# Kernel optimization log

Hardware: AMD Instinct MI355X
Metric: run time of the kernel (lower is better)

## Reference

```python
import jax, jax.numpy as jnp
import numpy as np

T, B, F, H, P = 256, 512, 256, 512, 12  # seq len, batch, feature_dim, hidden_dim, p_interval


def setup_inputs() -> dict:
    key = jax.random.key(0)
    ks = jax.random.split(key, 9)
    s = 1.0 / np.sqrt(F + H)  # torch Linear default init scale
    def lin(k):
        kw, kb = jax.random.split(k)
        W = jax.random.uniform(kw, (F + H, H), jnp.float32, -s, s)
        b = jax.random.uniform(kb, (H,), jnp.float32, -s, s)
        return W, b
    Wf, bf = lin(ks[0])
    Wi, bi = lin(ks[1])
    Wo, bo = lin(ks[2])
    Wg, bg = lin(ks[3])
    x = jax.random.normal(ks[4], (T, B, F), jnp.float32)
    return {"x": x, "Wf": Wf, "bf": bf, "Wi": Wi, "bi": bi,
            "Wo": Wo, "bo": bo, "Wg": Wg, "bg": bg}


def _slstm(x, Wf, bf, Wi, bi, Wo, bo, Wg, bg):
    Tn, Bn, _ = x.shape
    h0 = jnp.zeros((P, Bn, H), x.dtype)
    # NOTE: original torch code reassigns c to a 2D [B,H] tensor after step 0,
    # so c[t % P] indexes a batch ROW (shape [H]) that broadcasts. At t=0 the
    # slice is all-zeros either way, so carrying a 2D c is exactly faithful.
    c0 = jnp.zeros((Bn, H), x.dtype)

    def step(carry, inp):
        h, c = carry
        x_t, t = inp
        idx = t % P
        xc = jnp.concatenate([x_t, h[idx]], axis=1)  # [B, F+H]
        f = jax.nn.softmax(xc @ Wf + bf, axis=1)
        i = jax.nn.softmax(xc @ Wi + bi, axis=1)
        o = jax.nn.softmax(xc @ Wo + bo, axis=1)
        g = jnp.tanh(xc @ Wg + bg)
        c_new = jnp.tanh(f * c[idx] + i * g)  # c[idx]: row [H], broadcasts over B
        h = h.at[idx].set(o * c_new)
        return (h, c_new), None

    (h, _), _ = jax.lax.scan(step, (h0, c0), (x, jnp.arange(Tn)))
    return h[(Tn - 1) % P]


def reference(x, Wf, bf, Wi, bi, Wo, bo, Wg, bg):
    return _slstm(x, Wf, bf, Wi, bi, Wo, bo, Wg, bg)
```

## Files before the change

### kernel.cpp

```cpp
#include <hip/hip_runtime.h>

typedef unsigned short u16;
typedef unsigned int   u32;

typedef __attribute__((ext_vector_type(8))) short bf16x8;
typedef __attribute__((ext_vector_type(16))) float f32x16;

__device__ __forceinline__ u16 f2bf(float v) {
    u32 u = __float_as_uint(v);
    u32 r = (u + 0x7fffu + ((u >> 16) & 1u)) >> 16;
    return (u16)r;
}
__device__ __forceinline__ float bf2f(u16 h) { return __uint_as_float(((u32)h) << 16); }

__device__ __forceinline__ float ftanh(float x) {
    float e = __expf(2.0f * x);
    return 1.0f - 2.0f * __builtin_amdgcn_rcpf(e + 1.0f);
}

__device__ __forceinline__ void gl2lds16(const void* g, void* l) {
    __builtin_amdgcn_global_load_lds(
        (const __attribute__((address_space(1))) void*)g,
        (__attribute__((address_space(3))) void*)l, 16, 0, 0);
}

__global__ void init_k(u16* __restrict__ hh, u16* __restrict__ hl, float* __restrict__ cb) {
    int i = blockIdx.x * 256 + threadIdx.x;
    hh[i] = 0; hl[i] = 0;
    if (i < 2 * 512) cb[i] = 0.0f;
}

__global__ void pack_wq(const float* __restrict__ Wf, const float* __restrict__ bf_,
                        const float* __restrict__ Wi, const float* __restrict__ bi_,
                        const float* __restrict__ Wo, const float* __restrict__ bo_,
                        const float* __restrict__ Wg, const float* __restrict__ bg_,
                        u16* __restrict__ wq, float* __restrict__ bias4) {
    int idx = blockIdx.x * 256 + threadIdx.x;
    int n = idx / 768, k = idx - n * 768;
    int gate = n >> 9, col = n & 511;
    const float* W = (gate == 0) ? Wf : (gate == 1) ? Wi : (gate == 2) ? Wo : Wg;
    float v = W[k * 512 + col];
    u16 h = f2bf(v);
    u16 l = f2bf(v - bf2f(h));
    size_t base = (size_t)n * 2304;
    if (k < 256) {
        wq[base + k] = h; wq[base + 512 + k] = h; wq[base + 256 + k] = l;
    } else {
        int d = k - 256;
        wq[base + 768 + d] = h; wq[base + 1792 + d] = h; wq[base + 1280 + d] = l;
    }
    if (k == 0) {
        const float* bb = (gate == 0) ? bf_ : (gate == 1) ? bi_ : (gate == 2) ? bo_ : bg_;
        bias4[n] = bb[col];
    }
}

__global__ void split_x(const float* __restrict__ src, u16* __restrict__ oh, u16* __restrict__ ol) {
    int i = blockIdx.x * 256 + threadIdx.x;
    float4 v = ((const float4*)src)[i];
    u16 hx = f2bf(v.x), hy = f2bf(v.y), hz = f2bf(v.z), hw = f2bf(v.w);
    u16 lx = f2bf(v.x - bf2f(hx)), ly = f2bf(v.y - bf2f(hy));
    u16 lz = f2bf(v.z - bf2f(hz)), lw = f2bf(v.w - bf2f(hw));
    uint2 hv; hv.x = (u32)hx | ((u32)hy << 16); hv.y = (u32)hz | ((u32)hw << 16);
    uint2 lv; lv.x = (u32)lx | ((u32)ly << 16); lv.y = (u32)lz | ((u32)lw << 16);
    ((uint2*)oh)[i] = hv;
    ((uint2*)ol)[i] = lv;
}

#define KT 36
__global__ __launch_bounds__(512, 2) void gemm_q(
    const u16* __restrict__ xh, const u16* __restrict__ xl,
    const u16* __restrict__ hh, const u16* __restrict__ hl,
    const u16* __restrict__ wq, const float* __restrict__ bias4,
    float* __restrict__ lg, int Mvalid, int gx) {
    __shared__ __align__(16) u16 smem[69632];

    const int tid = threadIdx.x;
    const int wid = tid >> 6, lane = tid & 63;
    const int l32 = lane & 31, khalf = lane >> 5;
    const int wm = wid >> 2, wn = wid & 3;

    int bm, bn;
    if (gx == 32) { int xcd = blockIdx.x & 7, r = blockIdx.x >> 3; bm = xcd * 4 + (r & 3); bn = r >> 2; }
    else          { bm = blockIdx.x % gx; bn = blockIdx.x / gx; }

    const int lr8 = lane >> 3;
    const int ksw = ((lane & 7) ^ (lr8 & 7)) * 8;

    int arowc[3]; size_t brow[4];
#pragma unroll
    for (int c = 0; c < 3; ++c) {
        int row = bm * 192 + (wid * 3 + c) * 8 + lr8;
        if (row >= Mvalid) row = Mvalid - 1;
        arowc[c] = row;
    }
#pragma unroll
    for (int c = 0; c < 4; ++c)
        brow[c] = (size_t)(bn * 256 + (wid * 4 + c) * 8 + lr8) * 2304;

#define STAGE_A(kt, dstoff, c0, nc) do {                                      \
        int kt_ = (kt); const u16* base_; int str_, ko_;                      \
        if (kt_ < 12) { base_ = (kt_ >= 8) ? xl : xh; str_ = 256; ko_ = (kt_ & 3) * 64; } \
        else { int sub_ = kt_ - 12; base_ = (sub_ >= 16) ? hl : hh; str_ = 512; ko_ = (sub_ & 7) * 64; } \
        _Pragma("unroll")                                                     \
        for (int c_ = (c0); c_ < (c0) + (nc); ++c_)                           \
            gl2lds16(base_ + (size_t)arowc[c_] * str_ + ko_ + ksw,            \
                     smem + (dstoff) + (wid * 3 + c_) * 512 + lane * 8);      \
    } while (0)

#define STAGE_B(kt, dstoff, c0, nc) do {                                      \
        _Pragma("unroll")                                                     \
        for (int c_ = (c0); c_ < (c0) + (nc); ++c_)                           \
            gl2lds16(wq + brow[c_] + (kt) * 64 + ksw,                         \
                     smem + (dstoff) + (wid * 4 + c_) * 512 + lane * 8);      \
    } while (0)

    u32 offA[3][4], offB[2][4];
#pragma unroll
    for (int i = 0; i < 3; ++i) {
        int row = wm * 96 + i * 32 + l32;
        u32 rsw = (u32)(row & 7) << 3;
#pragma unroll
        for (int ks = 0; ks < 4; ++ks)
            offA[i][ks] = (u32)row * 64 + (((u32)(ks * 16 + khalf * 8)) ^ rsw);
    }
#pragma unroll
    for (int j = 0; j < 2; ++j) {
        int row = wn * 64 + j * 32 + l32;
        u32 rsw = (u32)(row & 7) << 3;
#pragma unroll
        for (int ks = 0; ks < 4; ++ks)
            offB[j][ks] = (u32)row * 64 + (((u32)(ks * 16 + khalf * 8)) ^ rsw);
    }

    f32x16 acc[3][2];
#pragma unroll
    for (int i = 0; i < 3; ++i)
#pragma unroll
        for (int j = 0; j < 2; ++j)
#pragma unroll
            for (int r = 0; r < 16; ++r) acc[i][j][r] = 0.f;

    STAGE_A(0, 0, 0, 3);
    STAGE_B(0, 36864, 0, 4);
    STAGE_A(1, 12288, 0, 3);
    asm volatile("s_waitcnt vmcnt(3)" ::: "memory");
    __builtin_amdgcn_s_barrier();
    __builtin_amdgcn_sched_barrier(0);

#pragma unroll 6
    for (int kt = 0; kt < KT; ++kt) {
        const u16* At = smem + (kt % 3) * 12288;
        const u16* Bt = smem + 36864 + (kt & 1) * 16384;
        const int bdst = 36864 + (((kt + 1) & 1) << 14);
        const int adst = ((kt + 2) % 3) * 12288;

#pragma unroll
        for (int p = 0; p < 4; ++p) {
            bf16x8 a[3], b[2];
#pragma unroll
            for (int i = 0; i < 3; ++i) a[i] = *(const bf16x8*)(At + offA[i][p]);
#pragma unroll
            for (int j = 0; j < 2; ++j) b[j] = *(const bf16x8*)(Bt + offB[j][p]);
            if (p == 0 && kt + 1 < KT) STAGE_B(kt + 1, bdst, 0, 2);
            if (p == 1 && kt + 1 < KT) STAGE_B(kt + 1, bdst, 2, 2);
            if (p == 2 && kt + 2 < KT) STAGE_A(kt + 2, adst, 0, 2);
            if (p == 3 && kt + 2 < KT) STAGE_A(kt + 2, adst, 2, 1);

            __builtin_amdgcn_s_barrier();
            __builtin_amdgcn_sched_barrier(0);

            __builtin_amdgcn_s_setprio(1);
#pragma unroll
            for (int i = 0; i < 3; ++i)
#pragma unroll
                for (int j = 0; j < 2; ++j)
                    acc[i][j] = __builtin_amdgcn_mfma_f32_32x32x16_bf16(a[i], b[j], acc[i][j], 0, 0, 0);
            __builtin_amdgcn_s_setprio(0);

            if (p < 3) {
                __builtin_amdgcn_s_barrier();
                __builtin_amdgcn_sched_barrier(0);
            }
        }

        if (kt < KT - 2) asm volatile("s_waitcnt vmcnt(3)" ::: "memory");
        else             asm volatile("s_waitcnt vmcnt(0)" ::: "memory");
        __builtin_amdgcn_s_barrier();
        __builtin_amdgcn_sched_barrier(0);
    }
#undef STAGE_A
#undef STAGE_B

#pragma unroll
    for (int j = 0; j < 2; ++j) {
        int n = bn * 256 + wn * 64 + j * 32 + l32;
        float bv = bias4[n];
#pragma unroll
        for (int i = 0; i < 3; ++i) {
            int rbase = bm * 192 + wm * 96 + i * 32 + 4 * khalf;
#pragma unroll
            for (int r = 0; r < 16; ++r) {
                int row = rbase + (r & 3) + 8 * (r >> 2);
                if (row < Mvalid)
                    lg[(size_t)row * 2048 + n] = acc[i][j][r] + bv;
            }
        }
    }
}

__device__ __forceinline__ void chain_step(const float* __restrict__ lg, int j, int lane, float r[8]) {
    int rowb = (j + 1) % 12;
    const float* base = lg + (size_t)(j * 512 + rowb) * 2048 + lane * 8;
    float f[8], iv[8], g[8];
#pragma unroll
    for (int u = 0; u < 8; ++u) { f[u] = base[u]; iv[u] = base[512 + u]; g[u] = base[1536 + u]; }
    float mf = -1e30f, mi = -1e30f;
#pragma unroll
    for (int u = 0; u < 8; ++u) { mf = fmaxf(mf, f[u]); mi = fmaxf(mi, iv[u]); }
#pragma unroll
    for (int o = 32; o; o >>= 1) { mf = fmaxf(mf, __shfl_xor(mf, o)); mi = fmaxf(mi, __shfl_xor(mi, o)); }
    float sf = 0.f, si = 0.f;
#pragma unroll
    for (int u = 0; u < 8; ++u) {
        f[u] = __expf(f[u] - mf); sf += f[u];
        iv[u] = __expf(iv[u] - mi); si += iv[u];
    }
#pragma unroll
    for (int o = 32; o; o >>= 1) { sf += __shfl_xor(sf, o); si += __shfl_xor(si, o); }
    float rf = __builtin_amdgcn_rcpf(sf), ri = __builtin_amdgcn_rcpf(si);
#pragma unroll
    for (int u = 0; u < 8; ++u) {
        float gg = ftanh(g[u]);
        r[u] = ftanh(f[u] * rf * r[u] + iv[u] * ri * gg);
    }
}

__global__ __launch_bounds__(256) void gates_k(
    const float* __restrict__ lg, float* __restrict__ cb,
    u16* __restrict__ hh, u16* __restrict__ hl,
    float* __restrict__ out, int t0, int S, int rd, int wr) {
    __shared__ float rsh[512];
    const int widx = threadIdx.x >> 6, lane = threadIdx.x & 63;
    const int s = (S - 1) - (blockIdx.x >> 7);
    const int b = (blockIdx.x & 127) * 4 + widx;
    const int t = t0 + s;

    if (widx == 0) {
        float r[8];
#pragma unroll
        for (int u = 0; u < 8; ++u) r[u] = cb[rd * 512 + lane * 8 + u];
        for (int j = 0; j < s; ++j) chain_step(lg, j, lane, r);
#pragma unroll
        for (int u = 0; u < 8; ++u) rsh[lane * 8 + u] = r[u];
        if ((int)blockIdx.x == 127 && t0 + S < 256) {
            chain_step(lg, S - 1, lane, r);
#pragma unroll
            for (int u = 0; u < 8; ++u) cb[wr * 512 + lane * 8 + u] = r[u];
        }
    }
    __syncthreads();

    const float* row = lg + (size_t)(s * 512 + b) * 2048 + lane * 8;
    float f[8], iv[8], ov[8], g[8];
#pragma unroll
    for (int u = 0; u < 8; ++u) {
        f[u] = row[u]; iv[u] = row[512 + u]; ov[u] = row[1024 + u]; g[u] = row[1536 + u];
    }
    float mf = -1e30f, mi = -1e30f, mo = -1e30f;
#pragma unroll
    for (int u = 0; u < 8; ++u) { mf = fmaxf(mf, f[u]); mi = fmaxf(mi, iv[u]); mo = fmaxf(mo, ov[u]); }
#pragma unroll
    for (int o = 32; o; o >>= 1) {
        mf = fmaxf(mf, __shfl_xor(mf, o));
        mi = fmaxf(mi, __shfl_xor(mi, o));
        mo = fmaxf(mo, __shfl_xor(mo, o));
    }
    float sf = 0.f, si = 0.f, so = 0.f;
#pragma unroll
    for (int u = 0; u < 8; ++u) {
        f[u] = __expf(f[u] - mf); sf += f[u];
        iv[u] = __expf(iv[u] - mi); si += iv[u];
        ov[u] = __expf(ov[u] - mo); so += ov[u];
    }
#pragma unroll
    for (int o = 32; o; o >>= 1) {
        sf += __shfl_xor(sf, o); si += __shfl_xor(si, o); so += __shfl_xor(so, o);
    }
    float rf = __builtin_amdgcn_rcpf(sf), ri = __builtin_amdgcn_rcpf(si), ro = __builtin_amdgcn_rcpf(so);
    float hout[8];
#pragma unroll
    for (int u = 0; u < 8; ++u) {
        float rr = rsh[lane * 8 + u];
        float gg = ftanh(g[u]);
        float cv = ftanh(f[u] * rf * rr + iv[u] * ri * gg);
        hout[u] = ov[u] * ro * cv;
    }
    u32 hhp[4], hlp[4];
#pragma unroll
    for (int u = 0; u < 4; ++u) {
        u16 h0 = f2bf(hout[2 * u]), h1 = f2bf(hout[2 * u + 1]);
        u16 l0 = f2bf(hout[2 * u] - bf2f(h0)), l1 = f2bf(hout[2 * u + 1] - bf2f(h1));
        hhp[u] = (u32)h0 | ((u32)h1 << 16);
        hlp[u] = (u32)l0 | ((u32)l1 << 16);
    }
    size_t hb = ((size_t)(s * 512 + b)) * 512 + lane * 8;
    *(uint4*)&hh[hb] = make_uint4(hhp[0], hhp[1], hhp[2], hhp[3]);
    *(uint4*)&hl[hb] = make_uint4(hlp[0], hlp[1], hlp[2], hlp[3]);
    if (t == 255) {
        float* op = out + (size_t)b * 512 + lane * 8;
#pragma unroll
        for (int u = 0; u < 8; ++u) op[u] = hout[u];
    }
}

extern "C" void kernel_launch(void* const* d_in, const int* in_sizes, int n_in,
                              void* d_out, int out_size, void* d_ws, size_t ws_size,
                              hipStream_t stream) {
    const float* x   = (const float*)d_in[0];
    const float* Wf  = (const float*)d_in[1];
    const float* bf_ = (const float*)d_in[2];
    const float* Wi  = (const float*)d_in[3];
    const float* bi_ = (const float*)d_in[4];
    const float* Wo  = (const float*)d_in[5];
    const float* bo_ = (const float*)d_in[6];
    const float* Wg  = (const float*)d_in[7];
    const float* bg_ = (const float*)d_in[8];
    float* out = (float*)d_out;

    char* p = (char*)d_ws;
    u16* xh  = (u16*)p; p += 134217728;
    u16* xl  = (u16*)p; p += 134217728;
    u16* wq  = (u16*)p; p += 9437184;
    u16* hh  = (u16*)p; p += 6291456;
    u16* hl  = (u16*)p; p += 6291456;
    float* bias4 = (float*)p; p += 8192;
    float* cb    = (float*)p; p += 4096;
    float* lg    = (float*)p; p += 50331648;

    init_k<<<12288, 256, 0, stream>>>(hh, hl, cb);
    pack_wq<<<6144, 256, 0, stream>>>(Wf, bf_, Wi, bi_, Wo, bo_, Wg, bg_, wq, bias4);
    split_x<<<32768, 256, 0, stream>>>(x, xh, xl);

    for (int blk = 0; blk < 22; ++blk) {
        int t0 = blk * 12;
        int S = (256 - t0 >= 12) ? 12 : (256 - t0);
        int M = S * 512;
        int gx = (M + 191) / 192;
        gemm_q<<<gx * 8, 512, 0, stream>>>(
            xh + (size_t)t0 * 512 * 256, xl + (size_t)t0 * 512 * 256,
            hh, hl, wq, bias4, lg, M, gx);
        gates_k<<<S * 128, 256, 0, stream>>>(lg, cb, hh, hl, out, t0, S, blk & 1, (blk + 1) & 1);
    }
}
```

Measured before the change: 1.988 ms.

## Software-pipeline LDS fragment reads against MFMAs and drop per-substep barriers

Replaces the four barrier-separated k-substeps in the GEMM main loop with a register-rotated schedule: LDS fragment reads for the next substep are issued before the MFMAs of the current one, and all global-to-LDS staging for the next tiles is issued up front in two bulk groups. The intra-iteration s_barriers are removed, leaving one barrier per k-tile, and builtin barriers become inline asm with memory clobbers. This is meant to hide LDS latency and cut synchronisation stalls. The cost is more live registers for the three fragment sets, which may reduce occupancy, and the schedule now depends on the compiler not reordering across the asm barriers.

New measurement: 1.991 ms. Within noise of the previous version (+0.1%).

```diff
diff --git a/kernel.cpp b/kernel.cpp
--- a/kernel.cpp
+++ b/kernel.cpp
@@ -98,19 +98,19 @@
     for (int c = 0; c < 4; ++c)
         brow[c] = (size_t)(bn * 256 + (wid * 4 + c) * 8 + lr8) * 2304;
 
-#define STAGE_A(kt, dstoff, c0, nc) do {                                      \
+#define STAGE_A(kt, dstoff) do {                                              \
         int kt_ = (kt); const u16* base_; int str_, ko_;                      \
         if (kt_ < 12) { base_ = (kt_ >= 8) ? xl : xh; str_ = 256; ko_ = (kt_ & 3) * 64; } \
         else { int sub_ = kt_ - 12; base_ = (sub_ >= 16) ? hl : hh; str_ = 512; ko_ = (sub_ & 7) * 64; } \
         _Pragma("unroll")                                                     \
-        for (int c_ = (c0); c_ < (c0) + (nc); ++c_)                           \
+        for (int c_ = 0; c_ < 3; ++c_)                                        \
             gl2lds16(base_ + (size_t)arowc[c_] * str_ + ko_ + ksw,            \
                      smem + (dstoff) + (wid * 3 + c_) * 512 + lane * 8);      \
     } while (0)
 
-#define STAGE_B(kt, dstoff, c0, nc) do {                                      \
+#define STAGE_B(kt, dstoff) do {                                              \
         _Pragma("unroll")                                                     \
-        for (int c_ = (c0); c_ < (c0) + (nc); ++c_)                           \
+        for (int c_ = 0; c_ < 4; ++c_)                                        \
             gl2lds16(wq + brow[c_] + (kt) * 64 + ksw,                         \
                      smem + (dstoff) + (wid * 4 + c_) * 512 + lane * 8);      \
     } while (0)
@@ -141,11 +141,29 @@
 #pragma unroll
             for (int r = 0; r < 16; ++r) acc[i][j][r] = 0.f;
 
-    STAGE_A(0, 0, 0, 3);
-    STAGE_B(0, 36864, 0, 4);
-    STAGE_A(1, 12288, 0, 3);
+#define RD(S, p) do {                                                         \
+        S##A0 = *(const bf16x8*)(At + offA[0][p]);                            \
+        S##A1 = *(const bf16x8*)(At + offA[1][p]);                            \
+        S##A2 = *(const bf16x8*)(At + offA[2][p]);                            \
+        S##B0 = *(const bf16x8*)(Bt + offB[0][p]);                            \
+        S##B1 = *(const bf16x8*)(Bt + offB[1][p]);                            \
+    } while (0)
+#define MM(S) do {                                                            \
+        __builtin_amdgcn_s_setprio(1);                                        \
+        acc[0][0] = __builtin_amdgcn_mfma_f32_32x32x16_bf16(S##A0, S##B0, acc[0][0], 0, 0, 0); \
+        acc[0][1] = __builtin_amdgcn_mfma_f32_32x32x16_bf16(S##A0, S##B1, acc[0][1], 0, 0, 0); \
+        acc[1][0] = __builtin_amdgcn_mfma_f32_32x32x16_bf16(S##A1, S##B0, acc[1][0], 0, 0, 0); \
+        acc[1][1] = __builtin_amdgcn_mfma_f32_32x32x16_bf16(S##A1, S##B1, acc[1][1], 0, 0, 0); \
+        acc[2][0] = __builtin_amdgcn_mfma_f32_32x32x16_bf16(S##A2, S##B0, acc[2][0], 0, 0, 0); \
+        acc[2][1] = __builtin_amdgcn_mfma_f32_32x32x16_bf16(S##A2, S##B1, acc[2][1], 0, 0, 0); \
+        __builtin_amdgcn_s_setprio(0);                                        \
+    } while (0)
+
+    STAGE_A(0, 0);
+    STAGE_B(0, 36864);
+    STAGE_A(1, 12288);
     asm volatile("s_waitcnt vmcnt(3)" ::: "memory");
-    __builtin_amdgcn_s_barrier();
+    asm volatile("s_barrier" ::: "memory");
     __builtin_amdgcn_sched_barrier(0);
 
 #pragma unroll 6
@@ -155,42 +173,30 @@
         const int bdst = 36864 + (((kt + 1) & 1) << 14);
         const int adst = ((kt + 2) % 3) * 12288;
 
-#pragma unroll
-        for (int p = 0; p < 4; ++p) {
-            bf16x8 a[3], b[2];
-#pragma unroll
-            for (int i = 0; i < 3; ++i) a[i] = *(const bf16x8*)(At + offA[i][p]);
-#pragma unroll
-            for (int j = 0; j < 2; ++j) b[j] = *(const bf16x8*)(Bt + offB[j][p]);
-            if (p == 0 && kt + 1 < KT) STAGE_B(kt + 1, bdst, 0, 2);
-            if (p == 1 && kt + 1 < KT) STAGE_B(kt + 1, bdst, 2, 2);
-            if (p == 2 && kt + 2 < KT) STAGE_A(kt + 2, adst, 0, 2);
-            if (p == 3 && kt + 2 < KT) STAGE_A(kt + 2, adst, 2, 1);
-
-            __builtin_amdgcn_s_barrier();
-            __builtin_amdgcn_sched_barrier(0);
-
-            __builtin_amdgcn_s_setprio(1);
-#pragma unroll
-            for (int i = 0; i < 3; ++i)
-#pragma unroll
-                for (int j = 0; j < 2; ++j)
-                    acc[i][j] = __builtin_amdgcn_mfma_f32_32x32x16_bf16(a[i], b[j], acc[i][j], 0, 0, 0);
-            __builtin_amdgcn_s_setprio(0);
-
-            if (p < 3) {
-                __builtin_amdgcn_s_barrier();
-                __builtin_amdgcn_sched_barrier(0);
-            }
-        }
+        bf16x8 saA0, saA1, saA2, saB0, saB1;
+        bf16x8 sbA0, sbA1, sbA2, sbB0, sbB1;
+        bf16x8 scA0, scA1, scA2, scB0, scB1;
+
+        RD(sa, 0);
+        if (kt + 1 < KT) STAGE_B(kt + 1, bdst);
+        RD(sb, 1);
+        if (kt + 2 < KT) STAGE_A(kt + 2, adst);
+        MM(sa);
+        RD(sc, 2);
+        MM(sb);
+        RD(sa, 3);
+        MM(sc);
+        MM(sa);
 
         if (kt < KT - 2) asm volatile("s_waitcnt vmcnt(3)" ::: "memory");
         else             asm volatile("s_waitcnt vmcnt(0)" ::: "memory");
-        __builtin_amdgcn_s_barrier();
+        asm volatile("s_barrier" ::: "memory");
         __builtin_amdgcn_sched_barrier(0);
     }
 #undef STAGE_A
 #undef STAGE_B
+#undef RD
+#undef MM
 
 #pragma unroll
     for (int j = 0; j < 2; ++j) {
```
